# Performance work log

Hardware: AMD Instinct MI355X
Metric: run time of the kernel (lower is better)

## Reference

```python
import jax, jax.numpy as jnp
import numpy as np

PATCH = 3  # patch_size=3, stride=1
B, C, H, W = 8, 256, 64, 64


def _extract_patches(x):
    # x: (c, h, w) -> (c*PATCH*PATCH, N) with N = (h-2)*(w-2), valid 3x3 patches
    c, h, w = x.shape
    hh, ww = h - PATCH + 1, w - PATCH + 1
    pats = jnp.stack([x[:, i:i + hh, j:j + ww]
                      for i in range(PATCH) for j in range(PATCH)], axis=0)  # (9, c, hh, ww)
    return pats.reshape(PATCH * PATCH * c, hh * ww)


def _index_to_flow(max_idx):
    # max_idx: (hh, ww) int -> flow (h, w, 2) padded by 2 at bottom/right
    hh, ww = max_idx.shape
    flow_w = (max_idx % ww).astype(jnp.float32)
    flow_h = (max_idx // ww).astype(jnp.float32)
    gy, gx = jnp.meshgrid(jnp.arange(hh, dtype=jnp.float32),
                          jnp.arange(ww, dtype=jnp.float32), indexing='ij')
    flow = jnp.stack((flow_w - gx, flow_h - gy), axis=2)  # (hh, ww, 2)
    return jnp.pad(flow, ((0, 2), (0, 2), (0, 0)))


def _per_image(feat_in, feat_ref):
    c, h, w = feat_in.shape
    hh, ww = h - PATCH + 1, w - PATCH + 1
    # channel-wise L2 normalize each spatial position (F.normalize dim=0, eps=1e-12)
    feat_in = feat_in / jnp.maximum(jnp.linalg.norm(feat_in, axis=0, keepdims=True), 1e-12)
    feat_ref = feat_ref / jnp.maximum(jnp.linalg.norm(feat_ref, axis=0, keepdims=True), 1e-12)
    Pi = _extract_patches(feat_in)    # (k, N)
    Pr = _extract_patches(feat_ref)   # (k, N)
    # is_norm=True: normalize ref patches (norm + 1e-5, per BasicSR feature_match_index)
    Pr = Pr / (jnp.linalg.norm(Pr, axis=0, keepdims=True) + 1e-5)
    corr = Pi.T @ Pr                  # (N, N) exhaustive patch correlation
    max_val = corr.max(axis=1)
    max_idx = jnp.argmax(corr, axis=1)
    # norm_input=True: divide by input patch norms
    max_val = max_val / jnp.linalg.norm(Pi, axis=0)
    max_val = max_val.reshape(hh, ww)
    max_idx = max_idx.reshape(hh, ww)
    sim = jnp.pad(max_val, ((1, 1), (1, 1)))[None]  # (1, h, w)
    flow = _index_to_flow(max_idx)                   # (h, w, 2)
    # nine down-right shifts (fill 0 at top-left), tensor_shift semantics
    shifted = jnp.stack([jnp.pad(flow[:h - i, :w - j], ((i, 0), (j, 0), (0, 0)))
                         for i in range(3) for j in range(3)], axis=0)  # (9, h, w, 2)
    return flow, shifted, sim


def setup_inputs() -> dict:
    key = jax.random.key(0)
    k1, k2 = jax.random.split(key)
    features1 = jax.random.normal(k1, (B, C, H, W), dtype=jnp.float32)
    features2 = jax.random.normal(k2, (B, C, H, W), dtype=jnp.float32)
    return {"features1": features1, "features2": features2}


def reference(features1, features2):
    pre_flow, pre_offset, pre_similarity = jax.vmap(_per_image)(features1, features2)
    # pre_flow: (b,h,w,2); pre_offset: (b,9,h,w,2); pre_similarity: (b,1,h,w)
    return pre_flow, pre_offset, pre_similarity
```

## Files before the change

kernel.cpp:

```cpp
#include <hip/hip_runtime.h>

typedef unsigned short u16;
typedef unsigned char u8;
typedef unsigned int u32;
typedef __bf16 bf16x8 __attribute__((ext_vector_type(8)));
typedef float f32x4 __attribute__((ext_vector_type(4)));

constexpr int BATCH = 8;
constexpr int C = 256;
constexpr int H = 64;
constexpr int W = 64;
constexpr int HW = H * W;
constexpr int HH = 62, WW = 62;
constexpr int NQ = HH * WW;
constexpr int SEG = 8;
constexpr int NBLK_RED = 536;

constexpr size_t OFF_RNORM = 0;
constexpr size_t OFF_RESV = 262144;
constexpr size_t OFF_RESI = 385280;
constexpr size_t OFF_SLOT0 = 508416;
constexpr size_t SP_H1 = 0;
constexpr size_t SP_L1 = 2097152;
constexpr size_t SP_H2 = 4194304;
constexpr size_t SP_L2 = 6291456;
constexpr size_t SP_P = 8388608;
constexpr size_t SP_PIDX8 = 75497472;
constexpr size_t SLOT_BYTES = 77594624;

typedef const __attribute__((address_space(1))) unsigned int* gas_ptr;
typedef __attribute__((address_space(3))) unsigned int* las_ptr;
__device__ __forceinline__ void gl16(const void* g, void* l) {
  __builtin_amdgcn_global_load_lds((gas_ptr)g, (las_ptr)l, 16, 0, 0);
}

__device__ __forceinline__ int pre_of(int ki) {
  if (ki <= 62) return ki * (ki + 1) / 2;
  int r = 123 - ki;
  return 1953 + 1891 - r * (r + 1) / 2;
}

__global__ __launch_bounds__(256) void norm_kernel(const float* __restrict__ f1,
                                                   const float* __restrict__ f2,
                                                   float* __restrict__ rnorm) {
  int by = blockIdx.x;
  int tensor = blockIdx.y;
  const float* f = tensor ? f2 : f1;
  int b = by >> 6, y = by & 63;
  int x = threadIdx.x & 63;
  int cq = threadIdx.x >> 6;
  const float* base = f + ((size_t)b * C) * HW + y * W + x;
  float s = 0.f;
  for (int c = cq; c < C; c += 4) {
    float v = base[(size_t)c * HW];
    s = fmaf(v, v, s);
  }
  __shared__ float sm[4][64];
  sm[cq][x] = s;
  __syncthreads();
  if (threadIdx.x < 64) {
    float t = sm[0][x] + sm[1][x] + sm[2][x] + sm[3][x];
    float nrm = fmaxf(sqrtf(t), 1e-12f);
    rnorm[((size_t)tensor * BATCH + b) * HW + y * W + x] = 1.0f / nrm;
  }
}

__global__ __launch_bounds__(256) void convert_kernel(const float* __restrict__ f1,
                                                      const float* __restrict__ f2,
                                                      const float* __restrict__ rnorm,
                                                      int b0, char* __restrict__ slot0) {
  int chunk = blockIdx.x;
  int tensor = blockIdx.y;
  int sloti = blockIdx.z;
  int bi = b0 + sloti;
  char* slot = slot0 + (size_t)sloti * SLOT_BYTES;
  int pos0 = chunk * 32;
  const float* f = (tensor ? f2 : f1) + (size_t)bi * C * HW;
  const float* rn = rnorm + ((size_t)tensor * BATCH + bi) * HW + pos0;
  u16* dh = (u16*)(slot + (tensor ? SP_H2 : SP_H1)) + (size_t)pos0 * C;
  u16* dl = (u16*)(slot + (tensor ? SP_L2 : SP_L1)) + (size_t)pos0 * C;

  __shared__ u32 sm[32][257];
  int t = threadIdx.x;
  int px = t & 31, cg = t >> 5;
  float r = rn[px];
  for (int kk = 0; kk < 32; ++kk) {
    int c = (cg << 5) + kk;
    float v = f[(size_t)c * HW + pos0 + px] * r;
    __bf16 h = (__bf16)v;
    float hf = (float)h;
    __bf16 lo = (__bf16)(v - hf);
    sm[px][c] = ((u32)__builtin_bit_cast(u16, h) << 16) | (u32)__builtin_bit_cast(u16, lo);
  }
  __syncthreads();
  int px2 = t >> 3, seg = t & 7;
  int c0 = seg * 32;
  for (int g8 = 0; g8 < 4; ++g8) {
    u32 hw0, hw1, hw2, hw3, lw0, lw1, lw2, lw3;
    u32 a, b2;
    a = sm[px2][c0 + g8 * 8 + 0]; b2 = sm[px2][c0 + g8 * 8 + 1];
    hw0 = (a >> 16) | (b2 & 0xFFFF0000u); lw0 = (a & 0xFFFFu) | (b2 << 16);
    a = sm[px2][c0 + g8 * 8 + 2]; b2 = sm[px2][c0 + g8 * 8 + 3];
    hw1 = (a >> 16) | (b2 & 0xFFFF0000u); lw1 = (a & 0xFFFFu) | (b2 << 16);
    a = sm[px2][c0 + g8 * 8 + 4]; b2 = sm[px2][c0 + g8 * 8 + 5];
    hw2 = (a >> 16) | (b2 & 0xFFFF0000u); lw2 = (a & 0xFFFFu) | (b2 << 16);
    a = sm[px2][c0 + g8 * 8 + 6]; b2 = sm[px2][c0 + g8 * 8 + 7];
    hw3 = (a >> 16) | (b2 & 0xFFFF0000u); lw3 = (a & 0xFFFFu) | (b2 << 16);
    size_t off = (size_t)px2 * C + c0 + g8 * 8;
    uint4 hv; hv.x = hw0; hv.y = hw1; hv.z = hw2; hv.w = hw3;
    uint4 lv; lv.x = lw0; lv.y = lw1; lv.z = lw2; lv.w = lw3;
    *(uint4*)(dh + off) = hv;
    *(uint4*)(dl + off) = lv;
  }
}

__global__ __launch_bounds__(256, 2) void pgemm_kernel(char* __restrict__ slot0) {
  char* slot = slot0 + (size_t)blockIdx.y * SLOT_BYTES;
  const u16* hi1 = (const u16*)(slot + SP_H1);
  const u16* lo1 = (const u16*)(slot + SP_L1);
  const u16* hi2 = (const u16*)(slot + SP_H2);
  const u16* lo2 = (const u16*)(slot + SP_L2);
  float* P = (float*)(slot + SP_P);

  int bid = blockIdx.x;
  int swz = (bid & 7) * 128 + (bid >> 3);
  int p0 = (swz >> 5) << 7, q0 = (swz & 31) << 7;

  __shared__ __align__(16) char smem[65536];

  int t = threadIdx.x;
  int l = t & 63, w = t >> 6, wm = w >> 1, wn = w & 1;
  int lr = l & 15, lh = l >> 4;

  const u16* srcs[4] = {hi1 + (size_t)p0 * 256, lo1 + (size_t)p0 * 256,
                        hi2 + (size_t)q0 * 256, lo2 + (size_t)q0 * 256};

  f32x4 acc[4][4];
#pragma unroll
  for (int mf = 0; mf < 4; ++mf)
#pragma unroll
    for (int nf = 0; nf < 4; ++nf)
      acc[mf][nf] = (f32x4){0.f, 0.f, 0.f, 0.f};

  auto stage = [&](int b, int kt) {
    char* base = smem + b * 32768;
#pragma unroll
    for (int pl = 0; pl < 4; ++pl) {
      const u16* s = srcs[pl];
#pragma unroll
      for (int wq = 0; wq < 2; ++wq) {
        int ci = (w * 2 + wq) * 64 + l;
        int row = ci >> 2, cc = ci & 3;
        size_t goff = (size_t)row * 256 + kt * 32 + ((cc ^ (row & 3)) << 3);
        gl16(s + goff, base + pl * 8192 + (w * 2 + wq) * 1024 + l * 16);
      }
    }
  };

  stage(0, 0);
  __syncthreads();

  for (int kt = 0; kt < 8; ++kt) {
    int b = kt & 1;
    if (kt < 7) stage(b ^ 1, kt + 1);
    char* sAh = smem + b * 32768;
    char* sAl = sAh + 8192;
    char* sBh = sAh + 16384;
    char* sBl = sAh + 24576;
    bf16x8 ah[4], al[4];
#pragma unroll
    for (int mf = 0; mf < 4; ++mf) {
      int row = wm * 64 + mf * 16 + lr;
      int off = row * 64 + (((lh) ^ (row & 3)) << 4);
      ah[mf] = *(const bf16x8*)(sAh + off);
      al[mf] = *(const bf16x8*)(sAl + off);
    }
#pragma unroll
    for (int nf = 0; nf < 4; ++nf) {
      int row = wn * 64 + nf * 16 + lr;
      int off = row * 64 + (((lh) ^ (row & 3)) << 4);
      bf16x8 bh = *(const bf16x8*)(sBh + off);
      bf16x8 bl = *(const bf16x8*)(sBl + off);
#pragma unroll
      for (int mf = 0; mf < 4; ++mf) {
        acc[mf][nf] = __builtin_amdgcn_mfma_f32_16x16x32_bf16(ah[mf], bh, acc[mf][nf], 0, 0, 0);
        acc[mf][nf] = __builtin_amdgcn_mfma_f32_16x16x32_bf16(al[mf], bh, acc[mf][nf], 0, 0, 0);
        acc[mf][nf] = __builtin_amdgcn_mfma_f32_16x16x32_bf16(ah[mf], bl, acc[mf][nf], 0, 0, 0);
      }
    }
    __syncthreads();
  }

  float* sq = (float*)smem;
#pragma unroll
  for (int pass = 0; pass < 2; ++pass) {
    if (pass) __syncthreads();
    if (wn == pass) {
      float* buf = sq + wm * 4352;
#pragma unroll
      for (int mf = 0; mf < 4; ++mf)
#pragma unroll
        for (int nf = 0; nf < 4; ++nf)
#pragma unroll
          for (int j = 0; j < 4; ++j)
            buf[(mf * 16 + lh * 4 + j) * 68 + nf * 16 + lr] = acc[mf][nf][j];
      *(f32x4*)(buf + l * 68 + 64) = (f32x4){0.f, 0.f, 0.f, 0.f};
    }
    __syncthreads();
    int tid2 = t & 127, sel = t >> 7;
    int ax = tid2 & 63, halfj = tid2 >> 6;
    const float* S = sq + sel * 4352;
    int rr1 = ax + 1 > 63 ? 63 : ax + 1;
    int rr2 = ax + 2 > 63 ? 63 : ax + 2;
    const float* S0 = S + ax * 68;
    const float* S1 = S + rr1 * 68;
    const float* S2 = S + rr2 * 68;
    int planeIdx = (((p0 >> 6) + sel) << 6) + (q0 >> 6) + pass;
    float* Qp = P + (((size_t)planeIdx) << 12);
#pragma unroll
    for (int gi = 0; gi < 4; ++gi) {
      int g = halfj * 4 + gi;
      int c0 = g * 8;
      float r0[12], r1a[12], r2a[12];
#pragma unroll
      for (int u = 0; u < 3; ++u) {
        *(f32x4*)(r0 + u * 4) = *(const f32x4*)(S0 + c0 + u * 4);
        *(f32x4*)(r1a + u * 4) = *(const f32x4*)(S1 + c0 + u * 4);
        *(f32x4*)(r2a + u * 4) = *(const f32x4*)(S2 + c0 + u * 4);
      }
      f32x4 qv0, qv1;
#pragma unroll
      for (int e = 0; e < 4; ++e) qv0[e] = r0[e] + r1a[e + 1] + r2a[e + 2];
#pragma unroll
      for (int e = 0; e < 4; ++e) qv1[e] = r0[e + 4] + r1a[e + 5] + r2a[e + 6];
      float* Qg = Qp + g * 512 + (ax << 2);
      *(f32x4*)(Qg) = qv0;
      *(f32x4*)(Qg + 256) = qv1;
    }
  }
}

__global__ __launch_bounds__(512) void reduce_kernel(char* __restrict__ slot0,
                                                     size_t slotBytes) {
  int slot = blockIdx.y;
  char* sb = slot0 + (size_t)slot * slotBytes;
  const float* QT = (const float*)(sb + SP_P);
  float* pval8 = (float*)sb;
  u8* pidx8 = (u8*)(sb + SP_PIDX8);

  int bid = blockIdx.x;
  int ki = 0;
  for (ki = 0; ki < 123; ++ki) {
    int d = ki - 61; if (d < 0) d = -d;
    int ns = (62 - d + SEG - 1) / SEG;
    if (bid < ns) break;
    bid -= ns;
  }
  int k = ki - 61;
  int ystart = k < 0 ? -k : 0;
  int yend = k > 0 ? 61 - k : 61;
  int y0 = ystart + bid * SEG;
  int y1 = y0 + SEG; if (y1 > yend + 1) y1 = yend + 1;
  int sid0 = pre_of(ki) + (y0 - ystart);
  int pmax = yend + 2;

  int t = threadIdx.x;
  int w = t >> 6, l = t & 63;

  float A[8], B[8], P0[8], P1[8], P2[8];

  auto ld = [&](int p, float* D) {
    const float* gp = QT + (((size_t)((p << 6) + (p + k))) << 12) + (w << 9) + (l << 2);
    *(f32x4*)(D) = *(const f32x4*)(gp);
    *(f32x4*)(D + 4) = *(const f32x4*)(gp + 256);
  };

  auto candstep = [&](int y, const float* D0, const float* D1, const float* D2) {
    float best = __uint_as_float(0xFF800000u);
    int bbb = 0;
#pragma unroll
    for (int s = 0; s < 8; ++s) {
      float c = D0[s] + D1[s] + D2[s];
      bool valid = (w * 8 + s) <= 61;
      if (valid && c > best) { best = c; bbb = s; }
    }
    size_t o = (size_t)(sid0 + (y - y0)) * 512 + (w << 6) + l;
    pval8[o] = best;
    pidx8[o] = (u8)bbb;
  };

  ld(y0, A);
  ld(y0 + 1, B);
  ld(y0 + 2, P0);
  ld(y0 + 3 > pmax ? pmax : y0 + 3, P1);
  ld(y0 + 4 > pmax ? pmax : y0 + 4, P2);

  int y = y0;
  while (true) {
    candstep(y, A, B, P0);
#pragma unroll
    for (int s = 0; s < 8; ++s) { A[s] = B[s]; B[s] = P0[s]; }
    if (++y >= y1) break;
    ld(y + 4 > pmax ? pmax : y + 4, P0);
    candstep(y, A, B, P1);
#pragma unroll
    for (int s = 0; s < 8; ++s) { A[s] = B[s]; B[s] = P1[s]; }
    if (++y >= y1) break;
    ld(y + 4 > pmax ? pmax : y + 4, P1);
    candstep(y, A, B, P2);
#pragma unroll
    for (int s = 0; s < 8; ++s) { A[s] = B[s]; B[s] = P2[s]; }
    if (++y >= y1) break;
    ld(y + 4 > pmax ? pmax : y + 4, P2);
  }
}

__global__ __launch_bounds__(256) void combine_kernel(const char* __restrict__ slot0,
                                                      size_t slotBytes, int b0,
                                                      float* __restrict__ resv,
                                                      int* __restrict__ residx) {
  int q = blockIdx.x * 256 + threadIdx.x;
  if (q >= NQ) return;
  int slot = blockIdx.y;
  int b = b0 + slot;
  const char* sb = slot0 + (size_t)slot * slotBytes;
  const float* pval8 = (const float*)sb;
  const u8* pidx8 = (const u8*)(sb + SP_PIDX8);
  int y = q / 62, ax = q - y * 62;
  float best = __uint_as_float(0xFF800000u);
  int bjy = 0, bw = 0;
  for (int jy = 0; jy < 62; ++jy) {
    int ki = 61 + jy - y;
    int sid = pre_of(ki) + (y < jy ? y : jy);
    const float* p = pval8 + (size_t)sid * 512 + ax;
#pragma unroll
    for (int ww = 0; ww < 8; ++ww) {
      float v = p[ww << 6];
      if (v > best) { best = v; bjy = jy; bw = ww; }
    }
  }
  int kib = 61 + bjy - y;
  int sidb = pre_of(kib) + (y < bjy ? y : bjy);
  int bb = pidx8[(size_t)sidb * 512 + (bw << 6) + ax];
  resv[(size_t)b * NQ + q] = best;
  residx[(size_t)b * NQ + q] = bjy * 62 + bw * 8 + bb;
}

__global__ __launch_bounds__(256) void assemble_kernel(const float* __restrict__ res_val,
                                                       const int* __restrict__ res_idx,
                                                       float* __restrict__ out) {
  int gid = blockIdx.x * 256 + threadIdx.x;
  if (gid >= BATCH * HW) return;
  int b = gid >> 12;
  int y = (gid >> 6) & 63;
  int x = gid & 63;

  float* out_flow = out;
  float* out_off = out + (size_t)BATCH * HW * 2;
  float* out_sim = out + (size_t)BATCH * HW * 2 + (size_t)BATCH * 9 * HW * 2;

  auto flow_at = [&](int yy, int xx, float* fx, float* fy) {
    if (yy >= 0 && yy < HH && xx >= 0 && xx < WW) {
      int idx = res_idx[(size_t)b * NQ + yy * WW + xx];
      *fx = (float)(idx % WW - xx);
      *fy = (float)(idx / WW - yy);
    } else {
      *fx = 0.f;
      *fy = 0.f;
    }
  };

  float fx, fy;
  flow_at(y, x, &fx, &fy);
  size_t fo = ((size_t)b * HW + y * W + x) * 2;
  out_flow[fo + 0] = fx;
  out_flow[fo + 1] = fy;

#pragma unroll
  for (int sft = 0; sft < 9; ++sft) {
    int i = sft / 3, j = sft % 3;
    float ox, oy;
    flow_at(y - i, x - j, &ox, &oy);
    size_t o = (((size_t)b * 9 + sft) * HW + y * W + x) * 2;
    out_off[o + 0] = ox;
    out_off[o + 1] = oy;
  }

  float sim = 0.f;
  if (y >= 1 && y <= HH && x >= 1 && x <= WW) {
    float mv = res_val[(size_t)b * NQ + (y - 1) * WW + (x - 1)];
    sim = mv * (1.0f / ((3.0f + 1e-5f) * 3.0f));
  }
  out_sim[(size_t)b * HW + y * W + x] = sim;
}

extern "C" void kernel_launch(void* const* d_in, const int* in_sizes, int n_in,
                              void* d_out, int out_size, void* d_ws, size_t ws_size,
                              hipStream_t stream) {
  const float* f1 = (const float*)d_in[0];
  const float* f2 = (const float*)d_in[1];
  float* out = (float*)d_out;
  char* ws = (char*)d_ws;

  float* rnorm = (float*)(ws + OFF_RNORM);
  float* resv = (float*)(ws + OFF_RESV);
  int* residx = (int*)(ws + OFF_RESI);
  char* slot0 = ws + OFF_SLOT0;

  int nslots = 1;
  if (ws_size > OFF_SLOT0 + SLOT_BYTES) {
    size_t n = (ws_size - OFF_SLOT0) / SLOT_BYTES;
    nslots = n >= 8 ? 8 : (int)n;
    if (nslots < 1) nslots = 1;
  }

  norm_kernel<<<dim3(BATCH * H, 2), 256, 0, stream>>>(f1, f2, rnorm);

  for (int b0 = 0; b0 < BATCH; b0 += nslots) {
    int g = BATCH - b0 < nslots ? BATCH - b0 : nslots;
    convert_kernel<<<dim3(128, 2, g), 256, 0, stream>>>(f1, f2, rnorm, b0, slot0);
    pgemm_kernel<<<dim3(1024, g), 256, 0, stream>>>(slot0);
    reduce_kernel<<<dim3(NBLK_RED, g), 512, 0, stream>>>(slot0, SLOT_BYTES);
    combine_kernel<<<dim3(16, g), 256, 0, stream>>>(slot0, SLOT_BYTES, b0,
                                                    resv, residx);
  }

  int total = BATCH * HW;
  assemble_kernel<<<(total + 255) / 256, 256, 0, stream>>>(resv, residx, out);
}
```

Baseline: 540.7 us.

## Fuse patch GEMM and diagonal reduction into one per-diagonal kernel

Replaces the separate tiled correlation GEMM and the diagonal max-reduction with one kernel. Each block owns one diagonal offset between image rows and walks the rows in order. For each row pair it computes a 64x64 bf16-split MFMA tile, sums the 3x3 patch terms in a three-slot shared-memory ring, and writes per-segment max and argmax directly. This removes the large intermediate correlation buffer, which was written once and read back through global memory. In exchange the work per block becomes serial over rows, with many barriers per small tile. Diagonals also differ in length, so load is uneven; interleaving short and long diagonals in the block order only partly balances it.

```diff
diff --git a/kernel.cpp b/kernel.cpp
--- a/kernel.cpp
+++ b/kernel.cpp
@@ -13,8 +13,6 @@
 constexpr int HW = H * W;
 constexpr int HH = 62, WW = 62;
 constexpr int NQ = HH * WW;
-constexpr int SEG = 8;
-constexpr int NBLK_RED = 536;
 
 constexpr size_t OFF_RNORM = 0;
 constexpr size_t OFF_RESV = 262144;
@@ -24,9 +22,9 @@
 constexpr size_t SP_L1 = 2097152;
 constexpr size_t SP_H2 = 4194304;
 constexpr size_t SP_L2 = 6291456;
-constexpr size_t SP_P = 8388608;
-constexpr size_t SP_PIDX8 = 75497472;
-constexpr size_t SLOT_BYTES = 77594624;
+constexpr size_t SP_PVAL = 8388608;
+constexpr size_t SP_PIDX = 16261120;
+constexpr size_t SLOT_BYTES = 18350080;
 
 typedef const __attribute__((address_space(1))) unsigned int* gas_ptr;
 typedef __attribute__((address_space(3))) unsigned int* las_ptr;
@@ -114,204 +112,124 @@
   }
 }
 
-__global__ __launch_bounds__(256, 2) void pgemm_kernel(char* __restrict__ slot0) {
-  char* slot = slot0 + (size_t)blockIdx.y * SLOT_BYTES;
-  const u16* hi1 = (const u16*)(slot + SP_H1);
-  const u16* lo1 = (const u16*)(slot + SP_L1);
-  const u16* hi2 = (const u16*)(slot + SP_H2);
-  const u16* lo2 = (const u16*)(slot + SP_L2);
-  float* P = (float*)(slot + SP_P);
-
-  int bid = blockIdx.x;
-  int swz = (bid & 7) * 128 + (bid >> 3);
-  int p0 = (swz >> 5) << 7, q0 = (swz & 31) << 7;
-
-  __shared__ __align__(16) char smem[65536];
-
-  int t = threadIdx.x;
-  int l = t & 63, w = t >> 6, wm = w >> 1, wn = w & 1;
-  int lr = l & 15, lh = l >> 4;
-
-  const u16* srcs[4] = {hi1 + (size_t)p0 * 256, lo1 + (size_t)p0 * 256,
-                        hi2 + (size_t)q0 * 256, lo2 + (size_t)q0 * 256};
-
-  f32x4 acc[4][4];
-#pragma unroll
-  for (int mf = 0; mf < 4; ++mf)
-#pragma unroll
-    for (int nf = 0; nf < 4; ++nf)
-      acc[mf][nf] = (f32x4){0.f, 0.f, 0.f, 0.f};
-
-  auto stage = [&](int b, int kt) {
-    char* base = smem + b * 32768;
-#pragma unroll
-    for (int pl = 0; pl < 4; ++pl) {
-      const u16* s = srcs[pl];
-#pragma unroll
-      for (int wq = 0; wq < 2; ++wq) {
-        int ci = (w * 2 + wq) * 64 + l;
-        int row = ci >> 2, cc = ci & 3;
-        size_t goff = (size_t)row * 256 + kt * 32 + ((cc ^ (row & 3)) << 3);
-        gl16(s + goff, base + pl * 8192 + (w * 2 + wq) * 1024 + l * 16);
-      }
-    }
-  };
-
-  stage(0, 0);
-  __syncthreads();
-
-  for (int kt = 0; kt < 8; ++kt) {
-    int b = kt & 1;
-    if (kt < 7) stage(b ^ 1, kt + 1);
-    char* sAh = smem + b * 32768;
-    char* sAl = sAh + 8192;
-    char* sBh = sAh + 16384;
-    char* sBl = sAh + 24576;
-    bf16x8 ah[4], al[4];
-#pragma unroll
-    for (int mf = 0; mf < 4; ++mf) {
-      int row = wm * 64 + mf * 16 + lr;
-      int off = row * 64 + (((lh) ^ (row & 3)) << 4);
-      ah[mf] = *(const bf16x8*)(sAh + off);
-      al[mf] = *(const bf16x8*)(sAl + off);
-    }
-#pragma unroll
-    for (int nf = 0; nf < 4; ++nf) {
-      int row = wn * 64 + nf * 16 + lr;
-      int off = row * 64 + (((lh) ^ (row & 3)) << 4);
-      bf16x8 bh = *(const bf16x8*)(sBh + off);
-      bf16x8 bl = *(const bf16x8*)(sBl + off);
-#pragma unroll
-      for (int mf = 0; mf < 4; ++mf) {
-        acc[mf][nf] = __builtin_amdgcn_mfma_f32_16x16x32_bf16(ah[mf], bh, acc[mf][nf], 0, 0, 0);
-        acc[mf][nf] = __builtin_amdgcn_mfma_f32_16x16x32_bf16(al[mf], bh, acc[mf][nf], 0, 0, 0);
-        acc[mf][nf] = __builtin_amdgcn_mfma_f32_16x16x32_bf16(ah[mf], bl, acc[mf][nf], 0, 0, 0);
-      }
-    }
-    __syncthreads();
-  }
-
-  float* sq = (float*)smem;
-#pragma unroll
-  for (int pass = 0; pass < 2; ++pass) {
-    if (pass) __syncthreads();
-    if (wn == pass) {
-      float* buf = sq + wm * 4352;
-#pragma unroll
-      for (int mf = 0; mf < 4; ++mf)
-#pragma unroll
-        for (int nf = 0; nf < 4; ++nf)
-#pragma unroll
-          for (int j = 0; j < 4; ++j)
-            buf[(mf * 16 + lh * 4 + j) * 68 + nf * 16 + lr] = acc[mf][nf][j];
-      *(f32x4*)(buf + l * 68 + 64) = (f32x4){0.f, 0.f, 0.f, 0.f};
-    }
-    __syncthreads();
-    int tid2 = t & 127, sel = t >> 7;
-    int ax = tid2 & 63, halfj = tid2 >> 6;
-    const float* S = sq + sel * 4352;
-    int rr1 = ax + 1 > 63 ? 63 : ax + 1;
-    int rr2 = ax + 2 > 63 ? 63 : ax + 2;
-    const float* S0 = S + ax * 68;
-    const float* S1 = S + rr1 * 68;
-    const float* S2 = S + rr2 * 68;
-    int planeIdx = (((p0 >> 6) + sel) << 6) + (q0 >> 6) + pass;
-    float* Qp = P + (((size_t)planeIdx) << 12);
-#pragma unroll
-    for (int gi = 0; gi < 4; ++gi) {
-      int g = halfj * 4 + gi;
-      int c0 = g * 8;
-      float r0[12], r1a[12], r2a[12];
-#pragma unroll
-      for (int u = 0; u < 3; ++u) {
-        *(f32x4*)(r0 + u * 4) = *(const f32x4*)(S0 + c0 + u * 4);
-        *(f32x4*)(r1a + u * 4) = *(const f32x4*)(S1 + c0 + u * 4);
-        *(f32x4*)(r2a + u * 4) = *(const f32x4*)(S2 + c0 + u * 4);
-      }
-      f32x4 qv0, qv1;
-#pragma unroll
-      for (int e = 0; e < 4; ++e) qv0[e] = r0[e] + r1a[e + 1] + r2a[e + 2];
-#pragma unroll
-      for (int e = 0; e < 4; ++e) qv1[e] = r0[e + 4] + r1a[e + 5] + r2a[e + 6];
-      float* Qg = Qp + g * 512 + (ax << 2);
-      *(f32x4*)(Qg) = qv0;
-      *(f32x4*)(Qg + 256) = qv1;
-    }
-  }
-}
-
-__global__ __launch_bounds__(512) void reduce_kernel(char* __restrict__ slot0,
-                                                     size_t slotBytes) {
-  int slot = blockIdx.y;
-  char* sb = slot0 + (size_t)slot * slotBytes;
-  const float* QT = (const float*)(sb + SP_P);
-  float* pval8 = (float*)sb;
-  u8* pidx8 = (u8*)(sb + SP_PIDX8);
-
-  int bid = blockIdx.x;
-  int ki = 0;
-  for (ki = 0; ki < 123; ++ki) {
-    int d = ki - 61; if (d < 0) d = -d;
-    int ns = (62 - d + SEG - 1) / SEG;
-    if (bid < ns) break;
-    bid -= ns;
-  }
+constexpr int QSLOT = 4160;
+
+__global__ __launch_bounds__(256, 2) void fused_kernel(char* __restrict__ slot0) {
+  int j = blockIdx.x;
+  int ki = (j & 1) ? (122 - (j >> 1)) : (j >> 1);
+  char* sb = slot0 + (size_t)blockIdx.y * SLOT_BYTES;
+  const u16* hi1 = (const u16*)(sb + SP_H1);
+  const u16* lo1 = (const u16*)(sb + SP_L1);
+  const u16* hi2 = (const u16*)(sb + SP_H2);
+  const u16* lo2 = (const u16*)(sb + SP_L2);
+  float* pval8 = (float*)(sb + SP_PVAL);
+  u8* pidx8 = (u8*)(sb + SP_PIDX);
+
   int k = ki - 61;
   int ystart = k < 0 ? -k : 0;
   int yend = k > 0 ? 61 - k : 61;
-  int y0 = ystart + bid * SEG;
-  int y1 = y0 + SEG; if (y1 > yend + 1) y1 = yend + 1;
-  int sid0 = pre_of(ki) + (y0 - ystart);
-  int pmax = yend + 2;
+  int sid0 = pre_of(ki);
+
+  __shared__ __align__(16) char buf0[16384];
+  __shared__ __align__(16) float qring[3 * QSLOT + 80];
 
   int t = threadIdx.x;
-  int w = t >> 6, l = t & 63;
-
-  float A[8], B[8], P0[8], P1[8], P2[8];
-
-  auto ld = [&](int p, float* D) {
-    const float* gp = QT + (((size_t)((p << 6) + (p + k))) << 12) + (w << 9) + (l << 2);
-    *(f32x4*)(D) = *(const f32x4*)(gp);
-    *(f32x4*)(D + 4) = *(const f32x4*)(gp + 256);
-  };
-
-  auto candstep = [&](int y, const float* D0, const float* D1, const float* D2) {
-    float best = __uint_as_float(0xFF800000u);
-    int bbb = 0;
-#pragma unroll
-    for (int s = 0; s < 8; ++s) {
-      float c = D0[s] + D1[s] + D2[s];
-      bool valid = (w * 8 + s) <= 61;
-      if (valid && c > best) { best = c; bbb = s; }
-    }
-    size_t o = (size_t)(sid0 + (y - y0)) * 512 + (w << 6) + l;
-    pval8[o] = best;
-    pidx8[o] = (u8)bbb;
-  };
-
-  ld(y0, A);
-  ld(y0 + 1, B);
-  ld(y0 + 2, P0);
-  ld(y0 + 3 > pmax ? pmax : y0 + 3, P1);
-  ld(y0 + 4 > pmax ? pmax : y0 + 4, P2);
-
-  int y = y0;
-  while (true) {
-    candstep(y, A, B, P0);
-#pragma unroll
-    for (int s = 0; s < 8; ++s) { A[s] = B[s]; B[s] = P0[s]; }
-    if (++y >= y1) break;
-    ld(y + 4 > pmax ? pmax : y + 4, P0);
-    candstep(y, A, B, P1);
-#pragma unroll
-    for (int s = 0; s < 8; ++s) { A[s] = B[s]; B[s] = P1[s]; }
-    if (++y >= y1) break;
-    ld(y + 4 > pmax ? pmax : y + 4, P1);
-    candstep(y, A, B, P2);
-#pragma unroll
-    for (int s = 0; s < 8; ++s) { A[s] = B[s]; B[s] = P2[s]; }
-    if (++y >= y1) break;
-    ld(y + 4 > pmax ? pmax : y + 4, P2);
+  int l = t & 63, w = t >> 6;
+  int lr = l & 15, lh = l >> 4;
+
+  int srow = t >> 2, ssl = t & 3;
+  int sq = ssl ^ ((srow >> 1) & 3);
+  size_t sgoff = (size_t)srow * 256 + sq * 8;
+
+  for (int r = ystart; r <= yend + 2; ++r) {
+    const u16* pa_h = hi1 + (size_t)(r << 6) * 256;
+    const u16* pa_l = lo1 + (size_t)(r << 6) * 256;
+    const u16* pb_h = hi2 + (size_t)((r + k) << 6) * 256;
+    const u16* pb_l = lo2 + (size_t)((r + k) << 6) * 256;
+    char* buf1 = (char*)&qring[(r % 3) * QSLOT];
+
+    f32x4 acc[4];
+#pragma unroll
+    for (int nf = 0; nf < 4; ++nf) acc[nf] = (f32x4){0.f, 0.f, 0.f, 0.f};
+
+    auto stage = [&](char* base, int kt) {
+      size_t go = sgoff + kt * 32;
+      gl16(pa_h + go, base + 0 + t * 16);
+      gl16(pa_l + go, base + 4096 + t * 16);
+      gl16(pb_h + go, base + 8192 + t * 16);
+      gl16(pb_l + go, base + 12288 + t * 16);
+    };
+
+    stage(buf0, 0);
+    __syncthreads();
+    for (int kt = 0; kt < 8; ++kt) {
+      char* sA = (kt & 1) ? buf1 : buf0;
+      if (kt < 7) stage((kt & 1) ? buf0 : buf1, kt + 1);
+      int arow = w * 16 + lr;
+      int aoff = arow * 64 + ((lh ^ ((arow >> 1) & 3)) << 4);
+      bf16x8 ah = *(const bf16x8*)(sA + aoff);
+      bf16x8 al = *(const bf16x8*)(sA + 4096 + aoff);
+#pragma unroll
+      for (int nf = 0; nf < 4; ++nf) {
+        int brow = nf * 16 + lr;
+        int boff = brow * 64 + ((lh ^ ((brow >> 1) & 3)) << 4);
+        bf16x8 bh = *(const bf16x8*)(sA + 8192 + boff);
+        bf16x8 bl = *(const bf16x8*)(sA + 12288 + boff);
+        acc[nf] = __builtin_amdgcn_mfma_f32_16x16x32_bf16(ah, bh, acc[nf], 0, 0, 0);
+        acc[nf] = __builtin_amdgcn_mfma_f32_16x16x32_bf16(al, bh, acc[nf], 0, 0, 0);
+        acc[nf] = __builtin_amdgcn_mfma_f32_16x16x32_bf16(ah, bl, acc[nf], 0, 0, 0);
+      }
+      __syncthreads();
+    }
+
+    float* T = &qring[(r % 3) * QSLOT];
+#pragma unroll
+    for (int nf = 0; nf < 4; ++nf)
+#pragma unroll
+      for (int jj = 0; jj < 4; ++jj)
+        T[(nf * 16 + lr) * 65 + w * 16 + lh * 4 + jj] = acc[nf][jj];
+    __syncthreads();
+
+    float qv[16];
+#pragma unroll
+    for (int i = 0; i < 16; ++i) {
+      int bx = i * 4 + w;
+      qv[i] = (bx <= 61)
+                  ? T[bx * 65 + l] + T[(bx + 1) * 65 + l + 1] + T[(bx + 2) * 65 + l + 2]
+                  : 0.f;
+    }
+    __syncthreads();
+#pragma unroll
+    for (int i = 0; i < 16; ++i) {
+      int bx = i * 4 + w;
+      if (bx <= 61) T[bx * 65 + l] = qv[i];
+    }
+    __syncthreads();
+
+    if (r >= ystart + 2) {
+      int y = r - 2;
+      const float* Q0 = &qring[((r - 2) % 3) * QSLOT];
+      const float* Q1 = &qring[((r - 1) % 3) * QSLOT];
+      const float* Q2 = T;
+#pragma unroll
+      for (int h = 0; h < 2; ++h) {
+        int ww = w * 2 + h;
+        float best = __uint_as_float(0xFF800000u);
+        int bbb = 0;
+#pragma unroll
+        for (int bb = 0; bb < 8; ++bb) {
+          int bx = ww * 8 + bb;
+          if (bx <= 61) {
+            float c = Q0[bx * 65 + l] + Q1[bx * 65 + l] + Q2[bx * 65 + l];
+            if (c > best) { best = c; bbb = bb; }
+          }
+        }
+        size_t o = (size_t)(sid0 + (y - ystart)) * 512 + (ww << 6) + l;
+        pval8[o] = best;
+        pidx8[o] = (u8)bbb;
+      }
+    }
+    __syncthreads();
   }
 }
 
@@ -324,8 +242,8 @@
   int slot = blockIdx.y;
   int b = b0 + slot;
   const char* sb = slot0 + (size_t)slot * slotBytes;
-  const float* pval8 = (const float*)sb;
-  const u8* pidx8 = (const u8*)(sb + SP_PIDX8);
+  const float* pval8 = (const float*)(sb + SP_PVAL);
+  const u8* pidx8 = (const u8*)(sb + SP_PIDX);
   int y = q / 62, ax = q - y * 62;
   float best = __uint_as_float(0xFF800000u);
   int bjy = 0, bw = 0;
@@ -378,9 +296,9 @@
 
 #pragma unroll
   for (int sft = 0; sft < 9; ++sft) {
-    int i = sft / 3, j = sft % 3;
+    int i = sft / 3, jj = sft % 3;
     float ox, oy;
-    flow_at(y - i, x - j, &ox, &oy);
+    flow_at(y - i, x - jj, &ox, &oy);
     size_t o = (((size_t)b * 9 + sft) * HW + y * W + x) * 2;
     out_off[o + 0] = ox;
     out_off[o + 1] = oy;
@@ -419,8 +337,7 @@
   for (int b0 = 0; b0 < BATCH; b0 += nslots) {
     int g = BATCH - b0 < nslots ? BATCH - b0 : nslots;
     convert_kernel<<<dim3(128, 2, g), 256, 0, stream>>>(f1, f2, rnorm, b0, slot0);
-    pgemm_kernel<<<dim3(1024, g), 256, 0, stream>>>(slot0);
-    reduce_kernel<<<dim3(NBLK_RED, g), 512, 0, stream>>>(slot0, SLOT_BYTES);
+    fused_kernel<<<dim3(123, g), 256, 0, stream>>>(slot0);
     combine_kernel<<<dim3(16, g), 256, 0, stream>>>(slot0, SLOT_BYTES, b0,
                                                     resv, residx);
   }
```

Result: slower. 756.9 us (+40.0%).
